# Kernel optimization log

Hardware: AMD Instinct MI355X
Metric: run time of the kernel (lower is better)

## Reference

```python
import jax, jax.numpy as jnp
import numpy as np

B, S, E, H = 4, 2048, 512, 8
DH = E // H
EPS = 1e-5

def _ln(x, g, b):
    m = jnp.mean(x, axis=-1, keepdims=True)
    v = jnp.var(x, axis=-1, keepdims=True)
    return (x - m) * jax.lax.rsqrt(v + EPS) * g + b

def setup_inputs() -> dict:
    key = jax.random.key(0)
    ks = jax.random.split(key, 8)
    sc = 0.02
    return {
        "x": jax.random.normal(ks[0], (B, S, E), dtype=jnp.float32),
        "ln1_g": jnp.ones((E,), jnp.float32),
        "ln1_b": jnp.zeros((E,), jnp.float32),
        "in_proj_w": sc * jax.random.normal(ks[1], (3 * E, E), jnp.float32),
        "in_proj_b": jnp.zeros((3 * E,), jnp.float32),
        "out_w": sc * jax.random.normal(ks[2], (E, E), jnp.float32),
        "out_b": jnp.zeros((E,), jnp.float32),
        "ln2_g": jnp.ones((E,), jnp.float32),
        "ln2_b": jnp.zeros((E,), jnp.float32),
        "fc1_w": sc * jax.random.normal(ks[3], (E, E), jnp.float32),
        "fc1_b": jnp.zeros((E,), jnp.float32),
        "fc2_w": sc * jax.random.normal(ks[4], (E, E), jnp.float32),
        "fc2_b": jnp.zeros((E,), jnp.float32),
    }

def reference(x, ln1_g, ln1_b, in_proj_w, in_proj_b, out_w, out_b,
              ln2_g, ln2_b, fc1_w, fc1_b, fc2_w, fc2_b):
    # pre-LN
    z = _ln(x, ln1_g, ln1_b)
    # qkv projection (torch MHA packed in_proj: [3E, E])
    qkv = z @ in_proj_w.T + in_proj_b          # [B,S,3E]
    q, k, v = jnp.split(qkv, 3, axis=-1)
    q = q.reshape(B, S, H, DH)
    k = k.reshape(B, S, H, DH)
    v = v.reshape(B, S, H, DH)
    scores = jnp.einsum("bqhd,bkhd->bhqk", q, k) / np.sqrt(DH).astype(np.float32)
    causal = jnp.triu(jnp.ones((S, S), dtype=bool), k=1)  # True = masked
    neg = jnp.finfo(scores.dtype).min
    scores = jnp.where(causal, neg, scores)
    attn = jax.nn.softmax(scores, axis=-1)      # [B,H,S,S]
    ctx = jnp.einsum("bhqk,bkhd->bqhd", attn, v).reshape(B, S, E)
    attn_out = ctx @ out_w.T + out_b
    # torch MHA with need_weights=True averages over heads by default
    attn_weights = jnp.mean(attn, axis=1)       # [B,S,S]
    z2 = x + attn_out
    y = _ln(z2, ln2_g, ln2_b)
    y = jax.nn.leaky_relu(y @ fc1_w.T + fc1_b, negative_slope=0.01)
    y = y @ fc2_w.T + fc2_b
    y = y + z2
    return (y, attn_weights)
```

## Files before the change

### kernel.cpp

```cpp
#include <hip/hip_runtime.h>

typedef short bf16x8 __attribute__((ext_vector_type(8)));
typedef float f32x4 __attribute__((ext_vector_type(4)));
typedef unsigned short u16x8 __attribute__((ext_vector_type(8)));

#define NB 4
#define SQ 2048
#define EM 512
#define NH 8
#define DHD 64
#define QSCALE 0.1803368801111731f

__device__ __forceinline__ unsigned short f2bf(float x) {
  unsigned u = __float_as_uint(x);
  u += 0x7FFFu + ((u >> 16) & 1u);
  return (unsigned short)(u >> 16);
}

__device__ __forceinline__ int sw8(int row, int col8) { return col8 ^ ((row & 7) << 3); }

__device__ __forceinline__ void glds16(const void* g, void* l) {
  __builtin_amdgcn_global_load_lds(
      (const __attribute__((address_space(1))) void*)g,
      (__attribute__((address_space(3))) void*)l, 16, 0, 0);
}

__global__ __launch_bounds__(256) void f2bf4_kernel(
    const float* __restrict__ w0, const float* __restrict__ w1,
    const float* __restrict__ w2, const float* __restrict__ w3,
    unsigned short* __restrict__ o0, unsigned short* __restrict__ o1,
    unsigned short* __restrict__ o2, unsigned short* __restrict__ o3) {
  int i = (blockIdx.x * 256 + threadIdx.x) * 8;
  const float* src;
  unsigned short* dst;
  int off;
  if (i < 786432) { src = w0; dst = o0; off = i; }
  else if (i < 1048576) { src = w1; dst = o1; off = i - 786432; }
  else if (i < 1310720) { src = w2; dst = o2; off = i - 1048576; }
  else { src = w3; dst = o3; off = i - 1310720; }
  f32x4 a = *(const f32x4*)(src + off);
  f32x4 b = *(const f32x4*)(src + off + 4);
  u16x8 o;
#pragma unroll
  for (int j = 0; j < 4; ++j) { o[j] = f2bf(a[j]); o[j + 4] = f2bf(b[j]); }
  *(u16x8*)(dst + off) = o;
}

__global__ __launch_bounds__(256) void ln_kernel(const float* __restrict__ x,
                                                 const float* __restrict__ g,
                                                 const float* __restrict__ bb,
                                                 unsigned short* __restrict__ out) {
  int tid = threadIdx.x;
  int row = blockIdx.x * 4 + (tid >> 6);
  int lane = tid & 63;
  size_t base = (size_t)row * EM + lane * 8;
  f32x4 v0 = *(const f32x4*)(x + base);
  f32x4 v1 = *(const f32x4*)(x + base + 4);
  float s = 0.f, q = 0.f;
#pragma unroll
  for (int j = 0; j < 4; ++j) { s += v0[j] + v1[j]; q += v0[j] * v0[j] + v1[j] * v1[j]; }
#pragma unroll
  for (int m = 1; m < 64; m <<= 1) { s += __shfl_xor(s, m); q += __shfl_xor(q, m); }
  float mean = s * (1.f / EM);
  float var = q * (1.f / EM) - mean * mean;
  float rs = rsqrtf(var + 1e-5f);
  f32x4 g0 = *(const f32x4*)(g + lane * 8), g1 = *(const f32x4*)(g + lane * 8 + 4);
  f32x4 b0 = *(const f32x4*)(bb + lane * 8), b1 = *(const f32x4*)(bb + lane * 8 + 4);
  u16x8 o;
#pragma unroll
  for (int j = 0; j < 4; ++j) {
    o[j] = f2bf((v0[j] - mean) * rs * g0[j] + b0[j]);
    o[j + 4] = f2bf((v1[j] - mean) * rs * g1[j] + b1[j]);
  }
  *(u16x8*)(out + base) = o;
}

template <bool LEAKY, bool RESID, bool OUTF32, bool QKV>
__global__ __launch_bounds__(256) void gemm64(
    const unsigned short* __restrict__ A, const unsigned short* __restrict__ Bm,
    const float* __restrict__ bias, const float* __restrict__ resid,
    float* __restrict__ outf, unsigned short* __restrict__ outh,
    unsigned short* __restrict__ qo, unsigned short* __restrict__ ko,
    unsigned short* __restrict__ vo, int M, int N, int K) {
  __shared__ unsigned short As[2][64][64];
  __shared__ unsigned short Bs[2][64][64];
  int m0 = blockIdx.x * 64, n0 = blockIdx.y * 64;
  int t = threadIdx.x;
  int wv = t >> 6, ln = t & 63, lg = ln >> 4, lr = ln & 15;
  int rsub = ln >> 3;
  int csw = ((ln & 7) ^ rsub) * 8;
  f32x4 acc[4];
#pragma unroll
  for (int c = 0; c < 4; ++c)
#pragma unroll
    for (int r = 0; r < 4; ++r) acc[c][r] = 0.f;

  const unsigned short* ag0 = A + (size_t)(m0 + wv * 16 + rsub) * K + csw;
  const unsigned short* ag1 = A + (size_t)(m0 + wv * 16 + 8 + rsub) * K + csw;
  const unsigned short* bg0 = Bm + (size_t)(n0 + wv * 16 + rsub) * K + csw;
  const unsigned short* bg1 = Bm + (size_t)(n0 + wv * 16 + 8 + rsub) * K + csw;

  glds16(ag0, &As[0][wv * 16][0]);
  glds16(ag1, &As[0][wv * 16 + 8][0]);
  glds16(bg0, &Bs[0][wv * 16][0]);
  glds16(bg1, &Bs[0][wv * 16 + 8][0]);

  int nk = K >> 6;
  for (int ki = 0; ki < nk; ++ki) {
    int cur = ki & 1;
    __syncthreads();
    if (ki + 1 < nk) {
      int nb = cur ^ 1;
      int ko_ = (ki + 1) * 64;
      glds16(ag0 + ko_, &As[nb][wv * 16][0]);
      glds16(ag1 + ko_, &As[nb][wv * 16 + 8][0]);
      glds16(bg0 + ko_, &Bs[nb][wv * 16][0]);
      glds16(bg1 + ko_, &Bs[nb][wv * 16 + 8][0]);
    }
#pragma unroll
    for (int kk = 0; kk < 64; kk += 32) {
      int arw = wv * 16 + lr;
      bf16x8 af = *(const bf16x8*)&As[cur][arw][sw8(arw, kk + lg * 8)];
#pragma unroll
      for (int c = 0; c < 4; ++c) {
        int brw = c * 16 + lr;
        bf16x8 bf = *(const bf16x8*)&Bs[cur][brw][sw8(brw, kk + lg * 8)];
        acc[c] = __builtin_amdgcn_mfma_f32_16x16x32_bf16(af, bf, acc[c], 0, 0, 0);
      }
    }
  }
#pragma unroll
  for (int c = 0; c < 4; ++c) {
    int C_ = n0 + c * 16 + lr;
    float bv = bias[C_];
#pragma unroll
    for (int r = 0; r < 4; ++r) {
      int R_ = m0 + wv * 16 + lg * 4 + r;
      float v = acc[c][r] + bv;
      if (LEAKY) v = v > 0.f ? v : 0.01f * v;
      if (RESID) v += resid[(size_t)R_ * N + C_];
      if (QKV) {
        int which = C_ >> 9, f = C_ & 511, h = f >> 6, d = f & 63;
        int b_ = R_ >> 11, s_ = R_ & 2047;
        if (which == 0) {
          qo[(((size_t)b_ * NH + h) * SQ + s_) * DHD + d] = f2bf(v * QSCALE);
        } else if (which == 1) {
          ko[(((size_t)b_ * NH + h) * SQ + s_) * DHD + d] = f2bf(v);
        } else {
          vo[(((size_t)b_ * NH + h) * DHD + d) * SQ + s_] = f2bf(v);
        }
      } else if (OUTF32) {
        outf[(size_t)R_ * N + C_] = v;
      } else {
        outh[(size_t)R_ * N + C_] = f2bf(v);
      }
    }
  }
}

template <bool QKV>
__global__ __launch_bounds__(256) void gemm128(
    const unsigned short* __restrict__ A, const unsigned short* __restrict__ Bm,
    const float* __restrict__ bias, unsigned short* __restrict__ qo,
    unsigned short* __restrict__ ko, unsigned short* __restrict__ vo,
    int M, int N, int K) {
  __shared__ unsigned short As[2][128][64];
  __shared__ unsigned short Bs[2][128][64];
  int m0 = blockIdx.x * 128, n0 = blockIdx.y * 128;
  int t = threadIdx.x;
  int wv = t >> 6, ln = t & 63, lg = ln >> 4, lr = ln & 15;
  int wr = wv >> 1, wc = wv & 1;
  int rsub = ln >> 3;
  int csw = ((ln & 7) ^ rsub) * 8;
  f32x4 acc[4][4];
#pragma unroll
  for (int m = 0; m < 4; ++m)
#pragma unroll
    for (int n = 0; n < 4; ++n)
#pragma unroll
      for (int r = 0; r < 4; ++r) acc[m][n][r] = 0.f;

  const unsigned short* agb = A + (size_t)(m0 + wv * 8 + rsub) * K + csw;
  const unsigned short* bgb = Bm + (size_t)(n0 + wv * 8 + rsub) * K + csw;

#pragma unroll
  for (int i = 0; i < 4; ++i) {
    glds16(agb + (size_t)(i * 32) * K, &As[0][i * 32 + wv * 8][0]);
    glds16(bgb + (size_t)(i * 32) * K, &Bs[0][i * 32 + wv * 8][0]);
  }

  int nk = K >> 6;
  for (int ki = 0; ki < nk; ++ki) {
    int cur = ki & 1;
    __syncthreads();
    if (ki + 1 < nk) {
      int nb = cur ^ 1;
      int ko_ = (ki + 1) * 64;
#pragma unroll
      for (int i = 0; i < 4; ++i) {
        glds16(agb + (size_t)(i * 32) * K + ko_, &As[nb][i * 32 + wv * 8][0]);
        glds16(bgb + (size_t)(i * 32) * K + ko_, &Bs[nb][i * 32 + wv * 8][0]);
      }
    }
#pragma unroll
    for (int kk = 0; kk < 64; kk += 32) {
      bf16x8 af[4], bfr[4];
#pragma unroll
      for (int m = 0; m < 4; ++m) {
        int arw = wr * 64 + m * 16 + lr;
        af[m] = *(const bf16x8*)&As[cur][arw][sw8(arw, kk + lg * 8)];
      }
#pragma unroll
      for (int n = 0; n < 4; ++n) {
        int brw = wc * 64 + n * 16 + lr;
        bfr[n] = *(const bf16x8*)&Bs[cur][brw][sw8(brw, kk + lg * 8)];
      }
#pragma unroll
      for (int m = 0; m < 4; ++m)
#pragma unroll
        for (int n = 0; n < 4; ++n)
          acc[m][n] = __builtin_amdgcn_mfma_f32_16x16x32_bf16(af[m], bfr[n], acc[m][n], 0, 0, 0);
    }
  }

#pragma unroll
  for (int n = 0; n < 4; ++n) {
    int C_ = n0 + wc * 64 + n * 16 + lr;
    float bv = bias[C_];
#pragma unroll
    for (int m = 0; m < 4; ++m) {
#pragma unroll
      for (int r = 0; r < 4; ++r) {
        int R_ = m0 + wr * 64 + m * 16 + lg * 4 + r;
        float v = acc[m][n][r] + bv;
        int which = C_ >> 9, f = C_ & 511, h = f >> 6, d = f & 63;
        int b_ = R_ >> 11, s_ = R_ & 2047;
        if (which == 0) {
          qo[(((size_t)b_ * NH + h) * SQ + s_) * DHD + d] = f2bf(v * QSCALE);
        } else if (which == 1) {
          ko[(((size_t)b_ * NH + h) * SQ + s_) * DHD + d] = f2bf(v);
        } else {
          vo[(((size_t)b_ * NH + h) * DHD + d) * SQ + s_] = f2bf(v);
        }
      }
    }
  }
}

__global__ __launch_bounds__(256) void flash_kernel(
    const unsigned short* __restrict__ Q, const unsigned short* __restrict__ Kb,
    const unsigned short* __restrict__ Vt, unsigned short* __restrict__ ctx,
    float* __restrict__ mstat, float* __restrict__ lstat) {
  __shared__ unsigned short Ks[2][64][64];
  __shared__ unsigned short Vs[2][64][64];
  __shared__ unsigned short Ps[4][16][64];
  int lin = blockIdx.x;
  int xcd = lin & 7, idx = lin >> 3;
  int qt = 31 - (idx >> 2);
  int grp = xcd + 8 * (idx & 3);
  int h = grp & 7, b = grp >> 3;
  int qb = qt * 64;
  int t = threadIdx.x, wv = t >> 6, ln = t & 63, lg = ln >> 4, lr = ln & 15;
  int rsub = ln >> 3;
  int csw = ((ln & 7) ^ rsub) * 8;
  size_t headoff = ((size_t)b * NH + h) * SQ;
  const unsigned short* kg0 = Kb + (headoff + wv * 16 + rsub) * DHD + csw;
  const unsigned short* kg1 = Kb + (headoff + wv * 16 + 8 + rsub) * DHD + csw;
  const unsigned short* vg0 = Vt + (((size_t)b * NH + h) * DHD + wv * 16 + rsub) * SQ + csw;
  const unsigned short* vg1 = Vt + (((size_t)b * NH + h) * DHD + wv * 16 + 8 + rsub) * SQ + csw;

  const unsigned short* qrow = Q + (headoff + qb + wv * 16 + lr) * DHD;
  bf16x8 aq0 = *(const bf16x8*)(qrow + lg * 8);
  bf16x8 aq1 = *(const bf16x8*)(qrow + 32 + lg * 8);

  bf16x8 vones;
#pragma unroll
  for (int j = 0; j < 8; ++j) vones[j] = (lr == 0) ? (short)0x3F80 : (short)0;

  f32x4 cacc[4], lacc;
#pragma unroll
  for (int nd = 0; nd < 4; ++nd)
#pragma unroll
    for (int r = 0; r < 4; ++r) cacc[nd][r] = 0.f;
#pragma unroll
  for (int r = 0; r < 4; ++r) lacc[r] = 0.f;
  float mrun[4];
#pragma unroll
  for (int r = 0; r < 4; ++r) mrun[r] = -__builtin_inff();

  int nkt = qt + 1;
  glds16(kg0, &Ks[0][wv * 16][0]);
  glds16(kg1, &Ks[0][wv * 16 + 8][0]);
  glds16(vg0, &Vs[0][wv * 16][0]);
  glds16(vg1, &Vs[0][wv * 16 + 8][0]);

  for (int kt = 0; kt < nkt; ++kt) {
    int cur = kt & 1;
    __syncthreads();
    if (kt + 1 < nkt) {
      int nb = cur ^ 1;
      size_t ko_ = (size_t)(kt + 1) * 64;
      glds16(kg0 + ko_ * DHD, &Ks[nb][wv * 16][0]);
      glds16(kg1 + ko_ * DHD, &Ks[nb][wv * 16 + 8][0]);
      glds16(vg0 + ko_, &Vs[nb][wv * 16][0]);
      glds16(vg1 + ko_, &Vs[nb][wv * 16 + 8][0]);
    }

    float sv[4][4];
    __builtin_amdgcn_s_setprio(1);
#pragma unroll
    for (int nt = 0; nt < 4; ++nt) {
      f32x4 sf;
#pragma unroll
      for (int r = 0; r < 4; ++r) sf[r] = 0.f;
      int brw = nt * 16 + lr;
      bf16x8 bk0 = *(const bf16x8*)&Ks[cur][brw][sw8(brw, lg * 8)];
      bf16x8 bk1 = *(const bf16x8*)&Ks[cur][brw][sw8(brw, 32 + lg * 8)];
      sf = __builtin_amdgcn_mfma_f32_16x16x32_bf16(aq0, bk0, sf, 0, 0, 0);
      sf = __builtin_amdgcn_mfma_f32_16x16x32_bf16(aq1, bk1, sf, 0, 0, 0);
#pragma unroll
      for (int r = 0; r < 4; ++r) sv[nt][r] = sf[r];
    }
    __builtin_amdgcn_s_setprio(0);
    if (kt == nkt - 1) {
      int kbase = kt * 64;
#pragma unroll
      for (int nt = 0; nt < 4; ++nt) {
        int kcol = kbase + nt * 16 + lr;
#pragma unroll
        for (int r = 0; r < 4; ++r) {
          int qr = qb + wv * 16 + lg * 4 + r;
          if (kcol > qr) sv[nt][r] = -__builtin_inff();
        }
      }
    }

    float lmax[4];
    bool need = false;
#pragma unroll
    for (int r = 0; r < 4; ++r) {
      lmax[r] = fmaxf(fmaxf(sv[0][r], sv[1][r]), fmaxf(sv[2][r], sv[3][r]));
      need |= (lmax[r] > mrun[r] + 8.f);
    }
    if (__any(need)) {
#pragma unroll
      for (int r = 0; r < 4; ++r) {
        float tm = lmax[r];
#pragma unroll
        for (int m = 1; m < 16; m <<= 1) tm = fmaxf(tm, __shfl_xor(tm, m));
        float mn = fmaxf(mrun[r], tm);
        float sc = exp2f(mrun[r] - mn);
        mrun[r] = mn;
        lacc[r] *= sc;
#pragma unroll
        for (int nd = 0; nd < 4; ++nd) cacc[nd][r] *= sc;
      }
    }
#pragma unroll
    for (int r = 0; r < 4; ++r) {
      int prow = lg * 4 + r;
#pragma unroll
      for (int nt = 0; nt < 4; ++nt) {
        float p = exp2f(sv[nt][r] - mrun[r]);
        Ps[wv][prow][sw8(prow, nt * 16 + lr)] =
            (unsigned short)(__float_as_uint(p) >> 16);
      }
    }

    bf16x8 pf0 = *(const bf16x8*)&Ps[wv][lr][sw8(lr, lg * 8)];
    bf16x8 pf1 = *(const bf16x8*)&Ps[wv][lr][sw8(lr, 32 + lg * 8)];
    __builtin_amdgcn_s_setprio(1);
    lacc = __builtin_amdgcn_mfma_f32_16x16x32_bf16(pf0, vones, lacc, 0, 0, 0);
    lacc = __builtin_amdgcn_mfma_f32_16x16x32_bf16(pf1, vones, lacc, 0, 0, 0);
#pragma unroll
    for (int nd = 0; nd < 4; ++nd) {
      int vrw = nd * 16 + lr;
      bf16x8 vf0 = *(const bf16x8*)&Vs[cur][vrw][sw8(vrw, lg * 8)];
      bf16x8 vf1 = *(const bf16x8*)&Vs[cur][vrw][sw8(vrw, 32 + lg * 8)];
      cacc[nd] = __builtin_amdgcn_mfma_f32_16x16x32_bf16(pf0, vf0, cacc[nd], 0, 0, 0);
      cacc[nd] = __builtin_amdgcn_mfma_f32_16x16x32_bf16(pf1, vf1, cacc[nd], 0, 0, 0);
    }
    __builtin_amdgcn_s_setprio(0);
  }

  float inv[4];
#pragma unroll
  for (int r = 0; r < 4; ++r) inv[r] = 1.f / __shfl(lacc[r], ln & 48);
#pragma unroll
  for (int nd = 0; nd < 4; ++nd)
#pragma unroll
    for (int r = 0; r < 4; ++r) {
      size_t dst = ((size_t)b * SQ + qb + wv * 16 + lg * 4 + r) * EM + h * DHD + nd * 16 + lr;
      ctx[dst] = f2bf(cacc[nd][r] * inv[r]);
    }
  if (lr == 0) {
#pragma unroll
    for (int r = 0; r < 4; ++r) {
      int row = qb + wv * 16 + lg * 4 + r;
      mstat[headoff + row] = mrun[r];
      lstat[headoff + row] = 0.125f * inv[r];
    }
  }
}

__global__ __launch_bounds__(256) void attnw_kernel(
    const unsigned short* __restrict__ Q, const unsigned short* __restrict__ Kb,
    const float* __restrict__ mstat, const float* __restrict__ lstat,
    float* __restrict__ aw) {
  int lin = blockIdx.x;
  int xcd = lin & 7, slot = lin >> 3;
  int combo = xcd + 8 * (slot >> 5);
  int qt = slot & 31;
  int kt2 = combo & 15, b = combo >> 4;
  int qb = qt * 64, kb = kt2 * 128;
  int t = threadIdx.x;
  float* tile = aw + ((size_t)b * SQ + qb) * SQ + kb;
  if (2 * kt2 > qt) {
    int row = t >> 2, cbase = (t & 3) * 32;
    f32x4 z;
#pragma unroll
    for (int j = 0; j < 4; ++j) z[j] = 0.f;
    float* p = tile + (size_t)row * SQ + cbase;
#pragma unroll
    for (int j = 0; j < 8; ++j) *(f32x4*)(p + j * 4) = z;
    return;
  }
  __shared__ unsigned short Ks[2][2][64][64];
  int wv = t >> 6, ln = t & 63, lg = ln >> 4, lr = ln & 15;
  int rsub = ln >> 3;
  int csw = ((ln & 7) ^ rsub) * 8;
  size_t khstride = (size_t)SQ * DHD;
  const unsigned short* kg00 = Kb + (((size_t)b * NH) * SQ + kb + wv * 16 + rsub) * DHD + csw;
  const unsigned short* kg01 = kg00 + (size_t)8 * DHD;
  const unsigned short* kg10 = kg00 + (size_t)64 * DHD;
  const unsigned short* kg11 = kg00 + (size_t)72 * DHD;
  const unsigned short* qg = Q + (((size_t)b * NH) * SQ + qb + wv * 16 + lr) * DHD + lg * 8;
  size_t mbase = (size_t)b * NH * SQ + qb + wv * 16 + lg * 4;

  glds16(kg00, &Ks[0][0][wv * 16][0]);
  glds16(kg01, &Ks[0][0][wv * 16 + 8][0]);
  glds16(kg10, &Ks[0][1][wv * 16][0]);
  glds16(kg11, &Ks[0][1][wv * 16 + 8][0]);

  bf16x8 aqc0 = *(const bf16x8*)qg;
  bf16x8 aqc1 = *(const bf16x8*)(qg + 32);
  bf16x8 aqn0 = *(const bf16x8*)(qg + khstride);
  bf16x8 aqn1 = *(const bf16x8*)(qg + khstride + 32);
  float mmc[4], lic[4], mmn[4], lin_[4];
#pragma unroll
  for (int r = 0; r < 4; ++r) {
    mmc[r] = mstat[mbase + r];
    lic[r] = lstat[mbase + r];
    mmn[r] = mstat[mbase + SQ + r];
    lin_[r] = lstat[mbase + SQ + r];
  }

  f32x4 facc[2][4];
#pragma unroll
  for (int j = 0; j < 2; ++j)
#pragma unroll
    for (int nt = 0; nt < 4; ++nt)
#pragma unroll
      for (int r = 0; r < 4; ++r) facc[j][nt][r] = 0.f;

  for (int h = 0; h < NH; ++h) {
    int cur = h & 1;
    __syncthreads();
    if (h + 1 < NH) {
      size_t ho = (size_t)(h + 1) * khstride;
      glds16(kg00 + ho, &Ks[cur ^ 1][0][wv * 16][0]);
      glds16(kg01 + ho, &Ks[cur ^ 1][0][wv * 16 + 8][0]);
      glds16(kg10 + ho, &Ks[cur ^ 1][1][wv * 16][0]);
      glds16(kg11 + ho, &Ks[cur ^ 1][1][wv * 16 + 8][0]);
    }

#pragma unroll
    for (int nt = 0; nt < 4; ++nt) {
      int brw = nt * 16 + lr;
      f32x4 sf0, sf1;
#pragma unroll
      for (int r = 0; r < 4; ++r) { sf0[r] = 0.f; sf1[r] = 0.f; }
      bf16x8 bk00 = *(const bf16x8*)&Ks[cur][0][brw][sw8(brw, lg * 8)];
      bf16x8 bk01 = *(const bf16x8*)&Ks[cur][0][brw][sw8(brw, 32 + lg * 8)];
      bf16x8 bk10 = *(const bf16x8*)&Ks[cur][1][brw][sw8(brw, lg * 8)];
      bf16x8 bk11 = *(const bf16x8*)&Ks[cur][1][brw][sw8(brw, 32 + lg * 8)];
      sf0 = __builtin_amdgcn_mfma_f32_16x16x32_bf16(aqc0, bk00, sf0, 0, 0, 0);
      sf1 = __builtin_amdgcn_mfma_f32_16x16x32_bf16(aqc0, bk10, sf1, 0, 0, 0);
      sf0 = __builtin_amdgcn_mfma_f32_16x16x32_bf16(aqc1, bk01, sf0, 0, 0, 0);
      sf1 = __builtin_amdgcn_mfma_f32_16x16x32_bf16(aqc1, bk11, sf1, 0, 0, 0);
#pragma unroll
      for (int r = 0; r < 4; ++r) {
        facc[0][nt][r] += exp2f(sf0[r] - mmc[r]) * lic[r];
        facc[1][nt][r] += exp2f(sf1[r] - mmc[r]) * lic[r];
      }
    }

    aqc0 = aqn0; aqc1 = aqn1;
#pragma unroll
    for (int r = 0; r < 4; ++r) { mmc[r] = mmn[r]; lic[r] = lin_[r]; }
    if (h + 2 < NH) {
      aqn0 = *(const bf16x8*)(qg + (size_t)(h + 2) * khstride);
      aqn1 = *(const bf16x8*)(qg + (size_t)(h + 2) * khstride + 32);
#pragma unroll
      for (int r = 0; r < 4; ++r) {
        mmn[r] = mstat[mbase + (size_t)(h + 2) * SQ + r];
        lin_[r] = lstat[mbase + (size_t)(h + 2) * SQ + r];
      }
    }
  }

#pragma unroll
  for (int j = 0; j < 2; ++j) {
    int ktj = 2 * kt2 + j;
    bool fullmask = (ktj > qt);
    bool dg = (ktj == qt);
#pragma unroll
    for (int nt = 0; nt < 4; ++nt) {
      int kc = kb + j * 64 + nt * 16 + lr;
#pragma unroll
      for (int r = 0; r < 4; ++r) {
        int qr = qb + wv * 16 + lg * 4 + r;
        float v = (fullmask || (dg && kc > qr)) ? 0.f : facc[j][nt][r];
        tile[(size_t)(wv * 16 + lg * 4 + r) * SQ + j * 64 + nt * 16 + lr] = v;
      }
    }
  }
}

extern "C" void kernel_launch(void* const* d_in, const int* in_sizes, int n_in,
                              void* d_out, int out_size, void* d_ws, size_t ws_size,
                              hipStream_t stream) {
  (void)in_sizes; (void)n_in; (void)out_size; (void)ws_size;
  const float* x = (const float*)d_in[0];
  const float* ln1g = (const float*)d_in[1];
  const float* ln1b = (const float*)d_in[2];
  const float* wqkv = (const float*)d_in[3];
  const float* bqkv = (const float*)d_in[4];
  const float* wout = (const float*)d_in[5];
  const float* bout = (const float*)d_in[6];
  const float* ln2g = (const float*)d_in[7];
  const float* ln2b = (const float*)d_in[8];
  const float* wfc1 = (const float*)d_in[9];
  const float* bfc1 = (const float*)d_in[10];
  const float* wfc2 = (const float*)d_in[11];
  const float* bfc2 = (const float*)d_in[12];

  char* ws = (char*)d_ws;
  unsigned short* zctx = (unsigned short*)(ws);
  unsigned short* qb_ = (unsigned short*)(ws + 8388608);
  unsigned short* kb_ = (unsigned short*)(ws + 16777216);
  unsigned short* vb_ = (unsigned short*)(ws + 25165824);
  float* z2 = (float*)(ws + 33554432);
  float* mstat = (float*)(ws + 50331648);
  float* lstat = (float*)(ws + 50593792);
  unsigned short* wqkv_h = (unsigned short*)(ws + 50855936);
  unsigned short* wout_h = (unsigned short*)(ws + 52428800);
  unsigned short* wfc1_h = (unsigned short*)(ws + 52953088);
  unsigned short* wfc2_h = (unsigned short*)(ws + 53477376);
  unsigned short* y1 = qb_;
  unsigned short* h1 = kb_;

  float* outy = (float*)d_out;
  float* outw = outy + (size_t)NB * SQ * EM;

  f2bf4_kernel<<<768, 256, 0, stream>>>(wqkv, wout, wfc1, wfc2,
                                        wqkv_h, wout_h, wfc1_h, wfc2_h);

  ln_kernel<<<2048, 256, 0, stream>>>(x, ln1g, ln1b, zctx);
  gemm128<true><<<dim3(64, 12), 256, 0, stream>>>(
      zctx, wqkv_h, bqkv, qb_, kb_, vb_, 8192, 1536, 512);
  flash_kernel<<<1024, 256, 0, stream>>>(qb_, kb_, vb_, zctx, mstat, lstat);
  attnw_kernel<<<2048, 256, 0, stream>>>(qb_, kb_, mstat, lstat, outw);
  gemm64<false, true, true, false><<<dim3(128, 8), 256, 0, stream>>>(
      zctx, wout_h, bout, x, z2, nullptr, nullptr, nullptr, nullptr, 8192, 512, 512);
  ln_kernel<<<2048, 256, 0, stream>>>(z2, ln2g, ln2b, y1);
  gemm64<true, false, false, false><<<dim3(128, 8), 256, 0, stream>>>(
      y1, wfc1_h, bfc1, nullptr, nullptr, h1, nullptr, nullptr, nullptr, 8192, 512, 512);
  gemm64<false, true, true, false><<<dim3(128, 8), 256, 0, stream>>>(
      h1, wfc2_h, bfc2, z2, outy, nullptr, nullptr, nullptr, nullptr, 8192, 512, 512);
}
```

Baseline: 176.8 us.

## Shrink QKV GEMM k-tile to 32, drop swizzle, add XCD-aware block mapping

The QKV projection GEMM now stages 128x32 k-slices instead of 128x64, halving shared memory per block and removing the XOR swizzle on LDS reads. The launch becomes a 1D grid remapped so the eight XCDs each own a contiguous band of M tiles, which should improve L2 reuse of A rows. A smaller LDS footprint may allow higher occupancy, but there are twice as many barrier iterations. Unswizzled 64-byte rows may also cause LDS bank conflicts.

```diff
diff --git a/kernel.cpp b/kernel.cpp
--- a/kernel.cpp
+++ b/kernel.cpp
@@ -158,20 +158,20 @@
   }
 }
 
-template <bool QKV>
-__global__ __launch_bounds__(256) void gemm128(
+__global__ __launch_bounds__(256) void gemm128qkv(
     const unsigned short* __restrict__ A, const unsigned short* __restrict__ Bm,
     const float* __restrict__ bias, unsigned short* __restrict__ qo,
-    unsigned short* __restrict__ ko, unsigned short* __restrict__ vo,
-    int M, int N, int K) {
-  __shared__ unsigned short As[2][128][64];
-  __shared__ unsigned short Bs[2][128][64];
-  int m0 = blockIdx.x * 128, n0 = blockIdx.y * 128;
+    unsigned short* __restrict__ ko, unsigned short* __restrict__ vo, int K) {
+  __shared__ unsigned short As[2][128][32];
+  __shared__ unsigned short Bs[2][128][32];
+  int lin = blockIdx.x;
+  int xcd = lin & 7, idx = lin >> 3;
+  int m0 = (xcd * 8 + (idx & 7)) * 128;
+  int n0 = (idx >> 3) * 128;
   int t = threadIdx.x;
   int wv = t >> 6, ln = t & 63, lg = ln >> 4, lr = ln & 15;
   int wr = wv >> 1, wc = wv & 1;
-  int rsub = ln >> 3;
-  int csw = ((ln & 7) ^ rsub) * 8;
+  int row16 = ln >> 2, chunk = (ln & 3) * 8;
   f32x4 acc[4][4];
 #pragma unroll
   for (int m = 0; m < 4; ++m)
@@ -180,47 +180,40 @@
 #pragma unroll
       for (int r = 0; r < 4; ++r) acc[m][n][r] = 0.f;
 
-  const unsigned short* agb = A + (size_t)(m0 + wv * 8 + rsub) * K + csw;
-  const unsigned short* bgb = Bm + (size_t)(n0 + wv * 8 + rsub) * K + csw;
-
-#pragma unroll
-  for (int i = 0; i < 4; ++i) {
-    glds16(agb + (size_t)(i * 32) * K, &As[0][i * 32 + wv * 8][0]);
-    glds16(bgb + (size_t)(i * 32) * K, &Bs[0][i * 32 + wv * 8][0]);
-  }
-
-  int nk = K >> 6;
+  const unsigned short* agA = A + (size_t)(m0 + wv * 16 + row16) * K + chunk;
+  const unsigned short* agB = A + (size_t)(m0 + 64 + wv * 16 + row16) * K + chunk;
+  const unsigned short* bgA = Bm + (size_t)(n0 + wv * 16 + row16) * K + chunk;
+  const unsigned short* bgB = Bm + (size_t)(n0 + 64 + wv * 16 + row16) * K + chunk;
+
+  glds16(agA, &As[0][wv * 16][0]);
+  glds16(agB, &As[0][64 + wv * 16][0]);
+  glds16(bgA, &Bs[0][wv * 16][0]);
+  glds16(bgB, &Bs[0][64 + wv * 16][0]);
+
+  int nk = K >> 5;
   for (int ki = 0; ki < nk; ++ki) {
     int cur = ki & 1;
     __syncthreads();
     if (ki + 1 < nk) {
       int nb = cur ^ 1;
-      int ko_ = (ki + 1) * 64;
-#pragma unroll
-      for (int i = 0; i < 4; ++i) {
-        glds16(agb + (size_t)(i * 32) * K + ko_, &As[nb][i * 32 + wv * 8][0]);
-        glds16(bgb + (size_t)(i * 32) * K + ko_, &Bs[nb][i * 32 + wv * 8][0]);
-      }
-    }
-#pragma unroll
-    for (int kk = 0; kk < 64; kk += 32) {
-      bf16x8 af[4], bfr[4];
-#pragma unroll
-      for (int m = 0; m < 4; ++m) {
-        int arw = wr * 64 + m * 16 + lr;
-        af[m] = *(const bf16x8*)&As[cur][arw][sw8(arw, kk + lg * 8)];
-      }
-#pragma unroll
-      for (int n = 0; n < 4; ++n) {
-        int brw = wc * 64 + n * 16 + lr;
-        bfr[n] = *(const bf16x8*)&Bs[cur][brw][sw8(brw, kk + lg * 8)];
-      }
-#pragma unroll
-      for (int m = 0; m < 4; ++m)
-#pragma unroll
-        for (int n = 0; n < 4; ++n)
-          acc[m][n] = __builtin_amdgcn_mfma_f32_16x16x32_bf16(af[m], bfr[n], acc[m][n], 0, 0, 0);
-    }
+      int ko_ = (ki + 1) * 32;
+      glds16(agA + ko_, &As[nb][wv * 16][0]);
+      glds16(agB + ko_, &As[nb][64 + wv * 16][0]);
+      glds16(bgA + ko_, &Bs[nb][wv * 16][0]);
+      glds16(bgB + ko_, &Bs[nb][64 + wv * 16][0]);
+    }
+    bf16x8 af[4], bfr[4];
+#pragma unroll
+    for (int m = 0; m < 4; ++m)
+      af[m] = *(const bf16x8*)&As[cur][wr * 64 + m * 16 + lr][lg * 8];
+#pragma unroll
+    for (int n = 0; n < 4; ++n)
+      bfr[n] = *(const bf16x8*)&Bs[cur][wc * 64 + n * 16 + lr][lg * 8];
+#pragma unroll
+    for (int m = 0; m < 4; ++m)
+#pragma unroll
+      for (int n = 0; n < 4; ++n)
+        acc[m][n] = __builtin_amdgcn_mfma_f32_16x16x32_bf16(af[m], bfr[n], acc[m][n], 0, 0, 0);
   }
 
 #pragma unroll
@@ -567,8 +560,7 @@
                                         wqkv_h, wout_h, wfc1_h, wfc2_h);
 
   ln_kernel<<<2048, 256, 0, stream>>>(x, ln1g, ln1b, zctx);
-  gemm128<true><<<dim3(64, 12), 256, 0, stream>>>(
-      zctx, wqkv_h, bqkv, qb_, kb_, vb_, 8192, 1536, 512);
+  gemm128qkv<<<768, 256, 0, stream>>>(zctx, wqkv_h, bqkv, qb_, kb_, vb_, 512);
   flash_kernel<<<1024, 256, 0, stream>>>(qb_, kb_, vb_, zctx, mstat, lstat);
   attnw_kernel<<<2048, 256, 0, stream>>>(qb_, kb_, mstat, lstat, outw);
   gemm64<false, true, true, false><<<dim3(128, 8), 256, 0, stream>>>(
```

Result: faster. 170.4 us (median of 2 runs) (-3.6%).
